# Performance work log

Measured on AMD Instinct MI355X. Metric: run time of the kernel, lower is better.

Reference implementation:

```python
import jax, jax.numpy as jnp
import numpy as np

N = 8192
F_IN = 128
N_META = 128
N_EMBED = 128


def setup_inputs() -> dict:
    key = jax.random.key(0)
    k1, k2, k3, k4, k5, k6 = jax.random.split(key, 6)
    X = jax.random.normal(k1, (N, F_IN), dtype=jnp.float32)
    A = jax.random.uniform(k2, (N, N), dtype=jnp.float32)  # dense nonneg adjacency
    s = 1.0 / np.sqrt(F_IN)
    W_embed = jax.random.uniform(k3, (N_EMBED, F_IN), dtype=jnp.float32, minval=-s, maxval=s)
    b_embed = jax.random.uniform(k4, (N_EMBED,), dtype=jnp.float32, minval=-s, maxval=s)
    W_assign = jax.random.uniform(k5, (N_META, F_IN), dtype=jnp.float32, minval=-s, maxval=s)
    b_assign = jax.random.uniform(k6, (N_META,), dtype=jnp.float32, minval=-s, maxval=s)
    return {"X": X, "A": A, "W_embed": W_embed, "b_embed": b_embed,
            "W_assign": W_assign, "b_assign": b_assign}


def reference(X, A, W_embed, b_embed, W_assign, b_assign):
    n = A.shape[0]
    # A_hat = A + I; symmetric normalization D^-1/2 A_hat D^-1/2.
    # (Original builds full diag matrices; result equals row/col scaling.)
    A_hat = A + jnp.eye(n, dtype=A.dtype)
    deg = jnp.sum(A_hat, axis=1)
    d_inv_sqrt = jnp.where(deg > 0, jax.lax.rsqrt(deg), 0.0)
    A_norm = d_inv_sqrt[:, None] * A_hat * d_inv_sqrt[None, :]
    AX = A_norm @ X  # shared by both GCN layers: [N, F]
    z_l = AX @ W_embed.T + b_embed                      # [N, n_embed]
    s_l = jax.nn.softmax(AX @ W_assign.T + b_assign, axis=-1)  # [N, n_meta]
    X_next = s_l.T @ z_l                                 # [n_meta, n_embed]
    A_next = s_l.T @ (A @ s_l)                           # [n_meta, n_meta]
    return (X_next, A_next, s_l)
```

## Files before the change

kernel.cpp:

```cpp
#include <hip/hip_runtime.h>
#include <hip/hip_bf16.h>
#include <cstdint>

typedef short v8s __attribute__((ext_vector_type(8)));
typedef float v4f __attribute__((ext_vector_type(4)));

#define DEV __device__ __forceinline__

DEV unsigned short f2bu(float f) {
  unsigned u = __builtin_bit_cast(unsigned, f);
  u += 0x7fffu + ((u >> 16) & 1u);
  return (unsigned short)(u >> 16);
}

DEV v8s pack8(const float4& a, const float4& b) {
  v8s r;
  r[0] = (short)f2bu(a.x); r[1] = (short)f2bu(a.y);
  r[2] = (short)f2bu(a.z); r[3] = (short)f2bu(a.w);
  r[4] = (short)f2bu(b.x); r[5] = (short)f2bu(b.y);
  r[6] = (short)f2bu(b.z); r[7] = (short)f2bu(b.w);
  return r;
}

template<bool CVT>
__global__ __launch_bounds__(256)
void k_degcvt(const float* __restrict__ A, float* __restrict__ dinv,
              unsigned short* __restrict__ Abf) {
  const int row = blockIdx.x;
  const float* ar = A + (size_t)row * 8192;
  unsigned short* aw = Abf + (size_t)row * 8192;
  float s = 0.f;
  #pragma unroll
  for (int i = 0; i < 8; ++i) {
    const int c = i * 1024 + threadIdx.x * 4;
    float4 v = *(const float4*)(ar + c);
    s += (v.x + v.y) + (v.z + v.w);
    if constexpr (CVT) {
      uint2 w;
      w.x = (unsigned)f2bu(v.x) | ((unsigned)f2bu(v.y) << 16);
      w.y = (unsigned)f2bu(v.z) | ((unsigned)f2bu(v.w) << 16);
      *(uint2*)(aw + c) = w;
    }
  }
  #pragma unroll
  for (int d = 1; d < 64; d <<= 1) s += __shfl_xor(s, d);
  __shared__ float wsum[4];
  if ((threadIdx.x & 63) == 0) wsum[threadIdx.x >> 6] = s;
  __syncthreads();
  if (threadIdx.x == 0) {
    dinv[row] = rsqrtf(1.0f + ((wsum[0] + wsum[1]) + (wsum[2] + wsum[3])));
  }
}

template<bool SCALE>
__global__ __launch_bounds__(256)
void k_transpose(const float* __restrict__ in, unsigned short* __restrict__ out,
                 const float* __restrict__ dinv) {
  __shared__ float tile[32][129];
  const int j0 = blockIdx.x * 32;
  const int t = threadIdx.x;
  const int r0 = t >> 5, sl = t & 31;
  #pragma unroll
  for (int i = 0; i < 4; ++i) {
    int r = r0 + i * 8;
    float4 v = *(const float4*)(in + (size_t)(j0 + r) * 128 + sl * 4);
    float sc = 1.0f;
    if constexpr (SCALE) sc = dinv[j0 + r];
    tile[r][sl * 4 + 0] = v.x * sc;
    tile[r][sl * 4 + 1] = v.y * sc;
    tile[r][sl * 4 + 2] = v.z * sc;
    tile[r][sl * 4 + 3] = v.w * sc;
  }
  __syncthreads();
  const int c = t >> 1, h = t & 1;
  unsigned short* op = out + (size_t)c * 8192 + j0 + h * 16;
  #pragma unroll
  for (int q = 0; q < 2; ++q) {
    int rb = h * 16 + q * 8;
    uint4 w;
    w.x = (unsigned)f2bu(tile[rb + 0][c]) | ((unsigned)f2bu(tile[rb + 1][c]) << 16);
    w.y = (unsigned)f2bu(tile[rb + 2][c]) | ((unsigned)f2bu(tile[rb + 3][c]) << 16);
    w.z = (unsigned)f2bu(tile[rb + 4][c]) | ((unsigned)f2bu(tile[rb + 5][c]) << 16);
    w.w = (unsigned)f2bu(tile[rb + 6][c]) | ((unsigned)f2bu(tile[rb + 7][c]) << 16);
    *(uint4*)(op + q * 8) = w;
  }
}

__global__ __launch_bounds__(512, 4)
void k_gemm_lds(const unsigned short* __restrict__ Ab16,
                const unsigned short* __restrict__ Bt, float* __restrict__ parts) {
  __shared__ alignas(16) char bsm[2][32768];
  const int t = threadIdx.x;
  const int wv = t >> 6, l = t & 63;
  const int rg = wv >> 1, wc = wv & 1;
  const int i0 = blockIdx.x * 128 + rg * 32;
  const int k0 = blockIdx.y * 1024;
  const int lr = l & 15, lq = l >> 4;

  const unsigned short* pA0 = Ab16 + (size_t)(i0 + lr) * 8192 + k0 + lq * 8;
  const unsigned short* pA1 = pA0 + (size_t)16 * 8192;

  const int sc = t >> 4, sk16 = t & 15;
  const unsigned short* pS = Bt + (size_t)sc * 8192 + k0 + sk16 * 8;
  int woff[4];
  #pragma unroll
  for (int i = 0; i < 4; ++i) {
    const int c = sc + i * 32;
    woff[i] = ((c << 8) + sk16 * 16) ^ ((c & 7) << 4);
  }

  v4f acc[2][4];
  #pragma unroll
  for (int mt = 0; mt < 2; ++mt)
    #pragma unroll
    for (int nt = 0; nt < 4; ++nt) acc[mt][nt] = (v4f){0.f, 0.f, 0.f, 0.f};

  v8s breg[4];
  v8s areg[2][4][2];

  auto stage_load = [&](int c) {
    #pragma unroll
    for (int i = 0; i < 4; ++i)
      breg[i] = *(const v8s*)(pS + (size_t)i * 32 * 8192 + c * 128);
  };
  auto stage_write = [&](int buf) {
    #pragma unroll
    for (int i = 0; i < 4; ++i)
      *(v8s*)(bsm[buf] + woff[i]) = breg[i];
  };

  stage_load(0);
  stage_write(0);
  #pragma unroll
  for (int kf = 0; kf < 4; ++kf) {
    areg[0][kf][0] = *(const v8s*)(pA0 + kf * 32);
    areg[0][kf][1] = *(const v8s*)(pA1 + kf * 32);
  }
  __syncthreads();

  #pragma unroll
  for (int c = 0; c < 8; ++c) {
    if (c < 7) {
      stage_load(c + 1);
      #pragma unroll
      for (int kf = 0; kf < 4; ++kf) {
        areg[(c + 1) & 1][kf][0] = *(const v8s*)(pA0 + (c + 1) * 128 + kf * 32);
        areg[(c + 1) & 1][kf][1] = *(const v8s*)(pA1 + (c + 1) * 128 + kf * 32);
      }
    }
    #pragma unroll
    for (int ks = 0; ks < 4; ++ks) {
      #pragma unroll
      for (int nt = 0; nt < 4; ++nt) {
        const int col = wc * 64 + nt * 16 + lr;
        const int off = (((col << 8) + ks * 64 + lq * 16) ^ ((col & 7) << 4));
        v8s bf = *(const v8s*)(bsm[c & 1] + off);
        acc[0][nt] = __builtin_amdgcn_mfma_f32_16x16x32_bf16(areg[c & 1][ks][0], bf, acc[0][nt], 0, 0, 0);
        acc[1][nt] = __builtin_amdgcn_mfma_f32_16x16x32_bf16(areg[c & 1][ks][1], bf, acc[1][nt], 0, 0, 0);
      }
    }
    if (c < 7) {
      stage_write((c + 1) & 1);
      __syncthreads();
    }
  }

  float* p = parts + (size_t)blockIdx.y * (8192 * 128);
  const int colb = wc * 64;
  #pragma unroll
  for (int mt = 0; mt < 2; ++mt)
    #pragma unroll
    for (int nt = 0; nt < 4; ++nt)
      #pragma unroll
      for (int r = 0; r < 4; ++r)
        p[(size_t)(i0 + mt * 16 + lq * 4 + r) * 128 + colb + nt * 16 + lr] = acc[mt][nt][r];
}

__global__ __launch_bounds__(512)
void k_gemm_f32(const float* __restrict__ Af, const unsigned short* __restrict__ Bt,
                float* __restrict__ parts) {
  constexpr int KSTEPS = 2048 / 32;
  const int t = threadIdx.x;
  const int wv = t >> 6, l = t & 63;
  const int rg = wv >> 1, ch = wv & 1;
  const int i0 = blockIdx.x * 128 + rg * 32;
  const int k0 = blockIdx.y * 2048;
  const int lr = l & 15, lk = (l >> 4) * 8;

  const float* pAf0 = Af + (size_t)(i0 + lr) * 8192 + k0 + lk;
  const float* pAf1 = pAf0 + (size_t)16 * 8192;
  const unsigned short* pB[4];
  #pragma unroll
  for (int nt = 0; nt < 4; ++nt)
    pB[nt] = Bt + (size_t)(ch * 64 + nt * 16 + lr) * 8192 + k0 + lk;

  v4f acc[2][4];
  #pragma unroll
  for (int mt = 0; mt < 2; ++mt)
    #pragma unroll
    for (int nt = 0; nt < 4; ++nt) acc[mt][nt] = (v4f){0.f, 0.f, 0.f, 0.f};

  float4 af_[2][2][2];
  v8s bb[2][4];

  auto loadab = [&](int buf, int k) {
    af_[buf][0][0] = *(const float4*)(pAf0 + k);
    af_[buf][0][1] = *(const float4*)(pAf0 + k + 4);
    af_[buf][1][0] = *(const float4*)(pAf1 + k);
    af_[buf][1][1] = *(const float4*)(pAf1 + k + 4);
    #pragma unroll
    for (int nt = 0; nt < 4; ++nt) bb[buf][nt] = *(const v8s*)(pB[nt] + k);
  };
  auto mfmas = [&](int buf) {
    #pragma unroll
    for (int mt = 0; mt < 2; ++mt) {
      v8s a_ = pack8(af_[buf][mt][0], af_[buf][mt][1]);
      #pragma unroll
      for (int nt = 0; nt < 4; ++nt)
        acc[mt][nt] = __builtin_amdgcn_mfma_f32_16x16x32_bf16(a_, bb[buf][nt], acc[mt][nt], 0, 0, 0);
    }
  };

  loadab(0, 0);
  for (int kt = 0; kt < KSTEPS; kt += 2) {
    loadab(1, (kt + 1) * 32);
    mfmas(0);
    if (kt + 2 < KSTEPS) loadab(0, (kt + 2) * 32);
    mfmas(1);
  }

  float* p = parts + (size_t)blockIdx.y * (8192 * 128);
  const int colb = ch * 64;
  #pragma unroll
  for (int mt = 0; mt < 2; ++mt)
    #pragma unroll
    for (int nt = 0; nt < 4; ++nt)
      #pragma unroll
      for (int r = 0; r < 4; ++r)
        p[(size_t)(i0 + mt * 16 + (l >> 4) * 4 + r) * 128 + colb + nt * 16 + lr] = acc[mt][nt][r];
}

__global__ __launch_bounds__(256)
void k_post1(const float* __restrict__ parts, int nsplit,
             const float* __restrict__ dinv, const float* __restrict__ Xg,
             const float* __restrict__ We, const float* __restrict__ be,
             const float* __restrict__ Wa, const float* __restrict__ ba,
             float* __restrict__ sl_out, unsigned short* __restrict__ slt,
             unsigned short* __restrict__ zlt) {
  __shared__ alignas(16) unsigned short axs[32 * 128];
  __shared__ float lg[32 * 128];
  __shared__ unsigned short sbf[32 * 130];
  __shared__ unsigned short zbf[32 * 130];
  const int t = threadIdx.x;
  const int i0 = blockIdx.x * 32;

  {
    const int r = t >> 3, cg = t & 7;
    const size_t base = (size_t)(i0 + r) * 128 + cg * 16;
    float acc[16];
    #pragma unroll
    for (int q = 0; q < 4; ++q) {
      float4 v = *(const float4*)(parts + base + q * 4);
      acc[q * 4 + 0] = v.x; acc[q * 4 + 1] = v.y;
      acc[q * 4 + 2] = v.z; acc[q * 4 + 3] = v.w;
    }
    for (int s = 1; s < nsplit; ++s) {
      #pragma unroll
      for (int q = 0; q < 4; ++q) {
        float4 v = *(const float4*)(parts + (size_t)s * 1048576 + base + q * 4);
        acc[q * 4 + 0] += v.x; acc[q * 4 + 1] += v.y;
        acc[q * 4 + 2] += v.z; acc[q * 4 + 3] += v.w;
      }
    }
    const float di = dinv[i0 + r];
    unsigned short bx[16];
    #pragma unroll
    for (int q = 0; q < 4; ++q) {
      float4 xv = *(const float4*)(Xg + base + q * 4);
      bx[q * 4 + 0] = f2bu(di * (acc[q * 4 + 0] + di * xv.x));
      bx[q * 4 + 1] = f2bu(di * (acc[q * 4 + 1] + di * xv.y));
      bx[q * 4 + 2] = f2bu(di * (acc[q * 4 + 2] + di * xv.z));
      bx[q * 4 + 3] = f2bu(di * (acc[q * 4 + 3] + di * xv.w));
    }
    char* Ab = (char*)axs;
    const int b0 = (r << 8) + cg * 32, sw = (r & 7) << 4;
    uint4 w0, w1;
    w0.x = (unsigned)bx[0] | ((unsigned)bx[1] << 16);
    w0.y = (unsigned)bx[2] | ((unsigned)bx[3] << 16);
    w0.z = (unsigned)bx[4] | ((unsigned)bx[5] << 16);
    w0.w = (unsigned)bx[6] | ((unsigned)bx[7] << 16);
    w1.x = (unsigned)bx[8] | ((unsigned)bx[9] << 16);
    w1.y = (unsigned)bx[10] | ((unsigned)bx[11] << 16);
    w1.z = (unsigned)bx[12] | ((unsigned)bx[13] << 16);
    w1.w = (unsigned)bx[14] | ((unsigned)bx[15] << 16);
    *(uint4*)(Ab + (b0 ^ sw)) = w0;
    *(uint4*)(Ab + ((b0 + 16) ^ sw)) = w1;
  }
  __syncthreads();

  const int wv = t >> 6, l = t & 63, fr = l & 15;
  {
    v4f zac[2][2], lac[2][2];
    #pragma unroll
    for (int a = 0; a < 2; ++a)
      #pragma unroll
      for (int b = 0; b < 2; ++b) {
        zac[a][b] = (v4f){0.f, 0.f, 0.f, 0.f};
        lac[a][b] = (v4f){0.f, 0.f, 0.f, 0.f};
      }
    const int kk = (l >> 4) * 8;
    #pragma unroll
    for (int ks = 0; ks < 4; ++ks) {
      const int k = ks * 32 + kk;
      #pragma unroll
      for (int nj = 0; nj < 2; ++nj) {
        const int col = nj * 64 + wv * 16 + fr;
        v8s bfe = pack8(*(const float4*)(We + col * 128 + k),
                        *(const float4*)(We + col * 128 + k + 4));
        v8s bfa = pack8(*(const float4*)(Wa + col * 128 + k),
                        *(const float4*)(Wa + col * 128 + k + 4));
        #pragma unroll
        for (int mt = 0; mt < 2; ++mt) {
          const int arow = mt * 16 + fr;
          v8s af = *(const v8s*)((char*)axs + (((arow << 8) + k * 2) ^ ((fr & 7) << 4)));
          zac[mt][nj] = __builtin_amdgcn_mfma_f32_16x16x32_bf16(af, bfe, zac[mt][nj], 0, 0, 0);
          lac[mt][nj] = __builtin_amdgcn_mfma_f32_16x16x32_bf16(af, bfa, lac[mt][nj], 0, 0, 0);
        }
      }
    }
    #pragma unroll
    for (int mt = 0; mt < 2; ++mt)
      #pragma unroll
      for (int nj = 0; nj < 2; ++nj)
        #pragma unroll
        for (int r4 = 0; r4 < 4; ++r4) {
          const int row = mt * 16 + (l >> 4) * 4 + r4;
          const int col = nj * 64 + wv * 16 + fr;
          lg[row * 128 + col] = lac[mt][nj][r4] + ba[col];
          zbf[row * 130 + col] = f2bu(zac[mt][nj][r4] + be[col]);
        }
  }
  __syncthreads();

  {
    const int r = t >> 3, g = t & 7;
    const float* lp = lg + r * 128 + g * 16;
    float x[16];
    #pragma unroll
    for (int q = 0; q < 4; ++q) {
      float4 v = *(const float4*)(lp + q * 4);
      x[q * 4 + 0] = v.x; x[q * 4 + 1] = v.y; x[q * 4 + 2] = v.z; x[q * 4 + 3] = v.w;
    }
    float mx = x[0];
    #pragma unroll
    for (int j = 1; j < 16; ++j) mx = fmaxf(mx, x[j]);
    #pragma unroll
    for (int d = 1; d < 8; d <<= 1) mx = fmaxf(mx, __shfl_xor(mx, d));
    float sum = 0.f;
    #pragma unroll
    for (int j = 0; j < 16; ++j) { x[j] = __expf(x[j] - mx); sum += x[j]; }
    #pragma unroll
    for (int d = 1; d < 8; d <<= 1) sum += __shfl_xor(sum, d);
    const float inv = 1.0f / sum;
    float* op = sl_out + (size_t)(i0 + r) * 128 + g * 16;
    #pragma unroll
    for (int q = 0; q < 4; ++q) {
      float4 o;
      o.x = x[q * 4 + 0] * inv; o.y = x[q * 4 + 1] * inv;
      o.z = x[q * 4 + 2] * inv; o.w = x[q * 4 + 3] * inv;
      *(float4*)(op + q * 4) = o;
    }
    #pragma unroll
    for (int j = 0; j < 16; ++j) sbf[r * 130 + g * 16 + j] = f2bu(x[j] * inv);
  }
  __syncthreads();

  {
    const int c = t & 127;
    const unsigned short* src = (t < 128) ? sbf : zbf;
    unsigned short* dst = (t < 128) ? slt : zlt;
    unsigned short* o = dst + (size_t)c * 8192 + i0;
    #pragma unroll
    for (int q = 0; q < 4; ++q) {
      uint4 w;
      w.x = (unsigned)src[(q * 8 + 0) * 130 + c] | ((unsigned)src[(q * 8 + 1) * 130 + c] << 16);
      w.y = (unsigned)src[(q * 8 + 2) * 130 + c] | ((unsigned)src[(q * 8 + 3) * 130 + c] << 16);
      w.z = (unsigned)src[(q * 8 + 4) * 130 + c] | ((unsigned)src[(q * 8 + 5) * 130 + c] << 16);
      w.w = (unsigned)src[(q * 8 + 6) * 130 + c] | ((unsigned)src[(q * 8 + 7) * 130 + c] << 16);
      *(uint4*)(o + q * 8) = w;
    }
  }
}

__global__ __launch_bounds__(256)
void k_post2(const float* __restrict__ parts, int nsplit, unsigned short* __restrict__ ast) {
  __shared__ unsigned short sb[32 * 130];
  const int t = threadIdx.x;
  const int i0 = blockIdx.x * 32;
  {
    const int r = t >> 3, cg = t & 7;
    const size_t base = (size_t)(i0 + r) * 128 + cg * 16;
    float acc[16];
    #pragma unroll
    for (int q = 0; q < 4; ++q) {
      float4 v = *(const float4*)(parts + base + q * 4);
      acc[q * 4 + 0] = v.x; acc[q * 4 + 1] = v.y;
      acc[q * 4 + 2] = v.z; acc[q * 4 + 3] = v.w;
    }
    for (int s = 1; s < nsplit; ++s) {
      #pragma unroll
      for (int q = 0; q < 4; ++q) {
        float4 v = *(const float4*)(parts + (size_t)s * 1048576 + base + q * 4);
        acc[q * 4 + 0] += v.x; acc[q * 4 + 1] += v.y;
        acc[q * 4 + 2] += v.z; acc[q * 4 + 3] += v.w;
      }
    }
    #pragma unroll
    for (int j = 0; j < 16; ++j) sb[r * 130 + cg * 16 + j] = f2bu(acc[j]);
  }
  __syncthreads();
  if (t < 128) {
    unsigned short* o = ast + (size_t)t * 8192 + i0;
    #pragma unroll
    for (int q = 0; q < 4; ++q) {
      uint4 w;
      w.x = (unsigned)sb[(q * 8 + 0) * 130 + t] | ((unsigned)sb[(q * 8 + 1) * 130 + t] << 16);
      w.y = (unsigned)sb[(q * 8 + 2) * 130 + t] | ((unsigned)sb[(q * 8 + 3) * 130 + t] << 16);
      w.z = (unsigned)sb[(q * 8 + 4) * 130 + t] | ((unsigned)sb[(q * 8 + 5) * 130 + t] << 16);
      w.w = (unsigned)sb[(q * 8 + 6) * 130 + t] | ((unsigned)sb[(q * 8 + 7) * 130 + t] << 16);
      *(uint4*)(o + q * 8) = w;
    }
  }
}

__global__ __launch_bounds__(256)
void k_outer(const unsigned short* __restrict__ slt, const unsigned short* __restrict__ zlt,
             const unsigned short* __restrict__ ast, float* __restrict__ parts) {
  const int t = threadIdx.x, wv = t >> 6, ln = t & 63;
  const int k0 = blockIdx.x * 128;
  const int lm = ln & 15, lk = (ln >> 4) << 3;
  v4f c1[2][8];
  v4f c2[2][8];
  #pragma unroll
  for (int mt = 0; mt < 2; ++mt)
    #pragma unroll
    for (int nt = 0; nt < 8; ++nt) { c1[mt][nt] = (v4f){0.f,0.f,0.f,0.f}; c2[mt][nt] = (v4f){0.f,0.f,0.f,0.f}; }
  #pragma unroll
  for (int ks = 0; ks < 4; ++ks) {
    int k = k0 + ks * 32 + lk;
    v8s a0 = *(const v8s*)(slt + (size_t)(wv * 32 + lm) * 8192 + k);
    v8s a1 = *(const v8s*)(slt + (size_t)(wv * 32 + 16 + lm) * 8192 + k);
    #pragma unroll
    for (int nt = 0; nt < 8; ++nt) {
      v8s bz = *(const v8s*)(zlt + (size_t)(nt * 16 + lm) * 8192 + k);
      v8s bs = *(const v8s*)(ast + (size_t)(nt * 16 + lm) * 8192 + k);
      c1[0][nt] = __builtin_amdgcn_mfma_f32_16x16x32_bf16(a0, bz, c1[0][nt], 0, 0, 0);
      c1[1][nt] = __builtin_amdgcn_mfma_f32_16x16x32_bf16(a1, bz, c1[1][nt], 0, 0, 0);
      c2[0][nt] = __builtin_amdgcn_mfma_f32_16x16x32_bf16(a0, bs, c2[0][nt], 0, 0, 0);
      c2[1][nt] = __builtin_amdgcn_mfma_f32_16x16x32_bf16(a1, bs, c2[1][nt], 0, 0, 0);
    }
  }
  float* p = parts + (size_t)blockIdx.x * 32768;
  #pragma unroll
  for (int mt = 0; mt < 2; ++mt)
    #pragma unroll
    for (int nt = 0; nt < 8; ++nt)
      #pragma unroll
      for (int r = 0; r < 4; ++r) {
        int m = wv * 32 + mt * 16 + ((ln >> 4) << 2) + r;
        int n = nt * 16 + lm;
        p[m * 128 + n] = c1[mt][nt][r];
        p[16384 + m * 128 + n] = c2[mt][nt][r];
      }
}

__global__ __launch_bounds__(256)
void k_reduce(const float* __restrict__ parts, float* __restrict__ out) {
  const int o = blockIdx.x * 256 + threadIdx.x;
  float s = 0.f;
  for (int b = 0; b < 64; ++b) s += parts[(size_t)b * 32768 + o];
  out[o] = s;
}

extern "C" void kernel_launch(void* const* d_in, const int* in_sizes, int n_in,
                              void* d_out, int out_size, void* d_ws, size_t ws_size,
                              hipStream_t stream) {
  (void)in_sizes; (void)n_in; (void)out_size;
  const float* X  = (const float*)d_in[0];
  const float* A  = (const float*)d_in[1];
  const float* We = (const float*)d_in[2];
  const float* be = (const float*)d_in[3];
  const float* Wa = (const float*)d_in[4];
  const float* ba = (const float*)d_in[5];
  float* out = (float*)d_out;
  float* sl = out + 32768;

  char* ws = (char*)d_ws;
  constexpr size_t OFF_XPT  = 32768;
  constexpr size_t OFF_SLT  = OFF_XPT + 2097152;
  constexpr size_t OFF_ZLT  = OFF_SLT + 2097152;
  constexpr size_t OFF_AST  = OFF_ZLT + 2097152;
  constexpr size_t OFF_PART = OFF_AST + 2097152;
  constexpr size_t OFF_ABF  = OFF_PART + 67108864;
  constexpr size_t NEED_ABF = OFF_ABF + 134217728ull;

  float*          dinv = (float*)(ws + 0);
  unsigned short* xpt  = (unsigned short*)(ws + OFF_XPT);
  unsigned short* slt  = (unsigned short*)(ws + OFF_SLT);
  unsigned short* zlt  = (unsigned short*)(ws + OFF_ZLT);
  unsigned short* ast  = (unsigned short*)(ws + OFF_AST);
  float*          part = (float*)(ws + OFF_PART);
  unsigned short* abfp = (unsigned short*)(ws + OFF_ABF);

  const bool abf = ws_size >= NEED_ABF;
  const int  sk  = abf ? 8 : 4;

  if (abf) k_degcvt<true><<<8192, 256, 0, stream>>>(A, dinv, abfp);
  else     k_degcvt<false><<<8192, 256, 0, stream>>>(A, dinv, abfp);

  k_transpose<true><<<256, 256, 0, stream>>>(X, xpt, dinv);

  if (abf) k_gemm_lds<<<dim3(64, 8), 512, 0, stream>>>(abfp, xpt, part);
  else     k_gemm_f32<<<dim3(64, 4), 512, 0, stream>>>(A, xpt, part);

  k_post1<<<256, 256, 0, stream>>>(part, sk, dinv, X, We, be, Wa, ba, sl, slt, zlt);

  if (abf) k_gemm_lds<<<dim3(64, 8), 512, 0, stream>>>(abfp, slt, part);
  else     k_gemm_f32<<<dim3(64, 4), 512, 0, stream>>>(A, slt, part);

  k_post2<<<256, 256, 0, stream>>>(part, sk, ast);
  k_outer<<<64, 256, 0, stream>>>(slt, zlt, ast, part);
  k_reduce<<<128, 256, 0, stream>>>(part, out);
}
```

Baseline: 203.8 us.

## Fuse split-K reduction and post-processing into GEMM via last-block atomic counter

The split-K GEMM now writes its partial sums as bf16 instead of fp32. An atomic counter per row-block picks the last finishing K-slice block, and that block reduces the eight partials and runs the epilogue in place: the dense projections, softmax and transposed stores for the first GEMM, and the transposed A·s store for the second. This removes the separate post1/post2 launches and halves the partial-sum traffic. In exchange, the epilogue runs on only 64 blocks, LDS use grows, and the bf16 partials add rounding error.

```diff
diff --git a/kernel.cpp b/kernel.cpp
--- a/kernel.cpp
+++ b/kernel.cpp
@@ -11,6 +11,10 @@
   unsigned u = __builtin_bit_cast(unsigned, f);
   u += 0x7fffu + ((u >> 16) & 1u);
   return (unsigned short)(u >> 16);
+}
+
+DEV float bu2f(unsigned short u) {
+  return __builtin_bit_cast(float, ((unsigned)u) << 16);
 }
 
 DEV v8s pack8(const float4& a, const float4& b) {
@@ -25,7 +29,8 @@
 template<bool CVT>
 __global__ __launch_bounds__(256)
 void k_degcvt(const float* __restrict__ A, float* __restrict__ dinv,
-              unsigned short* __restrict__ Abf) {
+              unsigned short* __restrict__ Abf, unsigned* __restrict__ cnt) {
+  if (blockIdx.x == 0 && threadIdx.x < 128) cnt[threadIdx.x] = 0;
   const int row = blockIdx.x;
   const float* ar = A + (size_t)row * 8192;
   unsigned short* aw = Abf + (size_t)row * 8192;
@@ -86,10 +91,20 @@
   }
 }
 
+template<int EPI>
 __global__ __launch_bounds__(512, 4)
 void k_gemm_lds(const unsigned short* __restrict__ Ab16,
-                const unsigned short* __restrict__ Bt, float* __restrict__ parts) {
-  __shared__ alignas(16) char bsm[2][32768];
+                const unsigned short* __restrict__ Bt,
+                unsigned short* __restrict__ parts, unsigned* __restrict__ cnt,
+                const float* __restrict__ dinv, const float* __restrict__ Xg,
+                const float* __restrict__ We, const float* __restrict__ be,
+                const float* __restrict__ Wa, const float* __restrict__ ba,
+                float* __restrict__ sl_out, unsigned short* __restrict__ slt,
+                unsigned short* __restrict__ zlt, unsigned short* __restrict__ ast) {
+  __shared__ alignas(16) char smem[66560];
+  __shared__ int lastf;
+  char* bsm0 = smem;
+  char* bsm1 = smem + 32768;
   const int t = threadIdx.x;
   const int wv = t >> 6, l = t & 63;
   const int rg = wv >> 1, wc = wv & 1;
@@ -123,14 +138,14 @@
     for (int i = 0; i < 4; ++i)
       breg[i] = *(const v8s*)(pS + (size_t)i * 32 * 8192 + c * 128);
   };
-  auto stage_write = [&](int buf) {
+  auto stage_write = [&](char* buf) {
     #pragma unroll
     for (int i = 0; i < 4; ++i)
-      *(v8s*)(bsm[buf] + woff[i]) = breg[i];
+      *(v8s*)(buf + woff[i]) = breg[i];
   };
 
   stage_load(0);
-  stage_write(0);
+  stage_write(bsm0);
   #pragma unroll
   for (int kf = 0; kf < 4; ++kf) {
     areg[0][kf][0] = *(const v8s*)(pA0 + kf * 32);
@@ -148,32 +163,218 @@
         areg[(c + 1) & 1][kf][1] = *(const v8s*)(pA1 + (c + 1) * 128 + kf * 32);
       }
     }
+    char* bcur = (c & 1) ? bsm1 : bsm0;
     #pragma unroll
     for (int ks = 0; ks < 4; ++ks) {
       #pragma unroll
       for (int nt = 0; nt < 4; ++nt) {
         const int col = wc * 64 + nt * 16 + lr;
         const int off = (((col << 8) + ks * 64 + lq * 16) ^ ((col & 7) << 4));
-        v8s bf = *(const v8s*)(bsm[c & 1] + off);
+        v8s bf = *(const v8s*)(bcur + off);
         acc[0][nt] = __builtin_amdgcn_mfma_f32_16x16x32_bf16(areg[c & 1][ks][0], bf, acc[0][nt], 0, 0, 0);
         acc[1][nt] = __builtin_amdgcn_mfma_f32_16x16x32_bf16(areg[c & 1][ks][1], bf, acc[1][nt], 0, 0, 0);
       }
     }
     if (c < 7) {
-      stage_write((c + 1) & 1);
+      stage_write((c & 1) ? bsm0 : bsm1);
       __syncthreads();
     }
   }
 
-  float* p = parts + (size_t)blockIdx.y * (8192 * 128);
-  const int colb = wc * 64;
-  #pragma unroll
-  for (int mt = 0; mt < 2; ++mt)
-    #pragma unroll
-    for (int nt = 0; nt < 4; ++nt)
-      #pragma unroll
-      for (int r = 0; r < 4; ++r)
-        p[(size_t)(i0 + mt * 16 + lq * 4 + r) * 128 + colb + nt * 16 + lr] = acc[mt][nt][r];
+  {
+    unsigned short* p = parts + (size_t)blockIdx.y * (8192 * 128);
+    const int colb = wc * 64;
+    #pragma unroll
+    for (int mt = 0; mt < 2; ++mt)
+      #pragma unroll
+      for (int nt = 0; nt < 4; ++nt)
+        #pragma unroll
+        for (int r = 0; r < 4; ++r)
+          p[(size_t)(i0 + mt * 16 + lq * 4 + r) * 128 + colb + nt * 16 + lr] = f2bu(acc[mt][nt][r]);
+  }
+
+  __threadfence();
+  if (t == 0) {
+    unsigned old = atomicAdd(&cnt[blockIdx.x], 1u);
+    lastf = (old == 7);
+  }
+  __syncthreads();
+  if (!lastf) return;
+  __threadfence();
+
+  const int i0g = blockIdx.x * 128;
+
+  if constexpr (EPI == 1) {
+    unsigned short* axs  = (unsigned short*)smem;
+    unsigned short* tbuf = (unsigned short*)(smem + 32768);
+
+    {
+      const int r = t >> 2, cg = t & 3;
+      const int gr = i0g + r;
+      float sacc[32];
+      #pragma unroll
+      for (int j = 0; j < 32; ++j) sacc[j] = 0.f;
+      for (int y = 0; y < 8; ++y) {
+        const unsigned short* pp = parts + (size_t)y * 1048576 + (size_t)gr * 128 + cg * 32;
+        #pragma unroll
+        for (int q = 0; q < 4; ++q) {
+          v8s v = *(const v8s*)(pp + q * 8);
+          #pragma unroll
+          for (int j = 0; j < 8; ++j)
+            sacc[q * 8 + j] += bu2f((unsigned short)v[j]);
+        }
+      }
+      const float di = dinv[gr];
+      const float* xp = Xg + (size_t)gr * 128 + cg * 32;
+      unsigned short ax[32];
+      #pragma unroll
+      for (int q = 0; q < 8; ++q) {
+        float4 xv = *(const float4*)(xp + q * 4);
+        ax[q * 4 + 0] = f2bu(di * (sacc[q * 4 + 0] + di * xv.x));
+        ax[q * 4 + 1] = f2bu(di * (sacc[q * 4 + 1] + di * xv.y));
+        ax[q * 4 + 2] = f2bu(di * (sacc[q * 4 + 2] + di * xv.z));
+        ax[q * 4 + 3] = f2bu(di * (sacc[q * 4 + 3] + di * xv.w));
+      }
+      char* axb = (char*)axs;
+      #pragma unroll
+      for (int u = 0; u < 4; ++u) {
+        uint4 w;
+        w.x = (unsigned)ax[u * 8 + 0] | ((unsigned)ax[u * 8 + 1] << 16);
+        w.y = (unsigned)ax[u * 8 + 2] | ((unsigned)ax[u * 8 + 3] << 16);
+        w.z = (unsigned)ax[u * 8 + 4] | ((unsigned)ax[u * 8 + 5] << 16);
+        w.w = (unsigned)ax[u * 8 + 6] | ((unsigned)ax[u * 8 + 7] << 16);
+        *(uint4*)(axb + (((r << 8) + cg * 64 + u * 16) ^ ((r & 7) << 4))) = w;
+      }
+    }
+    __syncthreads();
+
+    const int rb = wv * 16;
+    v4f zac[8], lac[8];
+    #pragma unroll
+    for (int nj = 0; nj < 8; ++nj) {
+      zac[nj] = (v4f){0.f, 0.f, 0.f, 0.f};
+      lac[nj] = (v4f){0.f, 0.f, 0.f, 0.f};
+    }
+    const char* axb = (const char*)axs;
+    #pragma unroll
+    for (int ks = 0; ks < 4; ++ks) {
+      const int k = ks * 32 + lq * 8;
+      const int arow = rb + lr;
+      v8s af = *(const v8s*)(axb + ((((arow) << 8) + k * 2) ^ ((lr & 7) << 4)));
+      #pragma unroll
+      for (int nj = 0; nj < 8; ++nj) {
+        const int cb = nj * 16 + lr;
+        v8s bfe = pack8(*(const float4*)(We + cb * 128 + k),
+                        *(const float4*)(We + cb * 128 + k + 4));
+        v8s bfa = pack8(*(const float4*)(Wa + cb * 128 + k),
+                        *(const float4*)(Wa + cb * 128 + k + 4));
+        zac[nj] = __builtin_amdgcn_mfma_f32_16x16x32_bf16(af, bfe, zac[nj], 0, 0, 0);
+        lac[nj] = __builtin_amdgcn_mfma_f32_16x16x32_bf16(af, bfa, lac[nj], 0, 0, 0);
+      }
+    }
+    #pragma unroll
+    for (int nj = 0; nj < 8; ++nj) {
+      const float bav = ba[nj * 16 + lr];
+      const float bev = be[nj * 16 + lr];
+      #pragma unroll
+      for (int r4 = 0; r4 < 4; ++r4) { lac[nj][r4] += bav; zac[nj][r4] += bev; }
+    }
+
+    #pragma unroll
+    for (int r4 = 0; r4 < 4; ++r4) {
+      float mx = lac[0][r4];
+      #pragma unroll
+      for (int nj = 1; nj < 8; ++nj) mx = fmaxf(mx, lac[nj][r4]);
+      #pragma unroll
+      for (int d = 1; d < 16; d <<= 1) mx = fmaxf(mx, __shfl_xor(mx, d));
+      float e[8], sum = 0.f;
+      #pragma unroll
+      for (int nj = 0; nj < 8; ++nj) { e[nj] = __expf(lac[nj][r4] - mx); sum += e[nj]; }
+      #pragma unroll
+      for (int d = 1; d < 16; d <<= 1) sum += __shfl_xor(sum, d);
+      const float inv = 1.0f / sum;
+      const int row = rb + lq * 4 + r4;
+      float* op = sl_out + (size_t)(i0g + row) * 128 + lr;
+      #pragma unroll
+      for (int nj = 0; nj < 8; ++nj) {
+        const float s = e[nj] * inv;
+        op[nj * 16] = s;
+        tbuf[row * 130 + nj * 16 + lr] = f2bu(s);
+      }
+    }
+    __syncthreads();
+
+    if (t < 128) {
+      unsigned short* o = slt + (size_t)t * 8192 + i0g;
+      #pragma unroll
+      for (int q = 0; q < 16; ++q) {
+        uint4 w;
+        w.x = (unsigned)tbuf[(q * 8 + 0) * 130 + t] | ((unsigned)tbuf[(q * 8 + 1) * 130 + t] << 16);
+        w.y = (unsigned)tbuf[(q * 8 + 2) * 130 + t] | ((unsigned)tbuf[(q * 8 + 3) * 130 + t] << 16);
+        w.z = (unsigned)tbuf[(q * 8 + 4) * 130 + t] | ((unsigned)tbuf[(q * 8 + 5) * 130 + t] << 16);
+        w.w = (unsigned)tbuf[(q * 8 + 6) * 130 + t] | ((unsigned)tbuf[(q * 8 + 7) * 130 + t] << 16);
+        *(uint4*)(o + q * 8) = w;
+      }
+    }
+    __syncthreads();
+
+    #pragma unroll
+    for (int nj = 0; nj < 8; ++nj)
+      #pragma unroll
+      for (int r4 = 0; r4 < 4; ++r4) {
+        const int row = rb + lq * 4 + r4;
+        tbuf[row * 130 + nj * 16 + lr] = f2bu(zac[nj][r4]);
+      }
+    __syncthreads();
+
+    if (t < 128) {
+      unsigned short* o = zlt + (size_t)t * 8192 + i0g;
+      #pragma unroll
+      for (int q = 0; q < 16; ++q) {
+        uint4 w;
+        w.x = (unsigned)tbuf[(q * 8 + 0) * 130 + t] | ((unsigned)tbuf[(q * 8 + 1) * 130 + t] << 16);
+        w.y = (unsigned)tbuf[(q * 8 + 2) * 130 + t] | ((unsigned)tbuf[(q * 8 + 3) * 130 + t] << 16);
+        w.z = (unsigned)tbuf[(q * 8 + 4) * 130 + t] | ((unsigned)tbuf[(q * 8 + 5) * 130 + t] << 16);
+        w.w = (unsigned)tbuf[(q * 8 + 6) * 130 + t] | ((unsigned)tbuf[(q * 8 + 7) * 130 + t] << 16);
+        *(uint4*)(o + q * 8) = w;
+      }
+    }
+  } else {
+    unsigned short* tbuf = (unsigned short*)smem;
+    {
+      const int r = t >> 2, cg = t & 3;
+      const int gr = i0g + r;
+      float sacc[32];
+      #pragma unroll
+      for (int j = 0; j < 32; ++j) sacc[j] = 0.f;
+      for (int y = 0; y < 8; ++y) {
+        const unsigned short* pp = parts + (size_t)y * 1048576 + (size_t)gr * 128 + cg * 32;
+        #pragma unroll
+        for (int q = 0; q < 4; ++q) {
+          v8s v = *(const v8s*)(pp + q * 8);
+          #pragma unroll
+          for (int j = 0; j < 8; ++j)
+            sacc[q * 8 + j] += bu2f((unsigned short)v[j]);
+        }
+      }
+      #pragma unroll
+      for (int j = 0; j < 32; ++j)
+        tbuf[r * 130 + cg * 32 + j] = f2bu(sacc[j]);
+    }
+    __syncthreads();
+    if (t < 128) {
+      unsigned short* o = ast + (size_t)t * 8192 + i0g;
+      #pragma unroll
+      for (int q = 0; q < 16; ++q) {
+        uint4 w;
+        w.x = (unsigned)tbuf[(q * 8 + 0) * 130 + t] | ((unsigned)tbuf[(q * 8 + 1) * 130 + t] << 16);
+        w.y = (unsigned)tbuf[(q * 8 + 2) * 130 + t] | ((unsigned)tbuf[(q * 8 + 3) * 130 + t] << 16);
+        w.z = (unsigned)tbuf[(q * 8 + 4) * 130 + t] | ((unsigned)tbuf[(q * 8 + 5) * 130 + t] << 16);
+        w.w = (unsigned)tbuf[(q * 8 + 6) * 130 + t] | ((unsigned)tbuf[(q * 8 + 7) * 130 + t] << 16);
+        *(uint4*)(o + q * 8) = w;
+      }
+    }
+  }
 }
 
 __global__ __launch_bounds__(512)
@@ -501,34 +702,42 @@
   constexpr size_t OFF_ZLT  = OFF_SLT + 2097152;
   constexpr size_t OFF_AST  = OFF_ZLT + 2097152;
   constexpr size_t OFF_PART = OFF_AST + 2097152;
+  constexpr size_t OFF_CNT  = OFF_PART + 33554432;
   constexpr size_t OFF_ABF  = OFF_PART + 67108864;
   constexpr size_t NEED_ABF = OFF_ABF + 134217728ull;
 
-  float*          dinv = (float*)(ws + 0);
-  unsigned short* xpt  = (unsigned short*)(ws + OFF_XPT);
-  unsigned short* slt  = (unsigned short*)(ws + OFF_SLT);
-  unsigned short* zlt  = (unsigned short*)(ws + OFF_ZLT);
-  unsigned short* ast  = (unsigned short*)(ws + OFF_AST);
-  float*          part = (float*)(ws + OFF_PART);
-  unsigned short* abfp = (unsigned short*)(ws + OFF_ABF);
+  float*          dinv  = (float*)(ws + 0);
+  unsigned short* xpt   = (unsigned short*)(ws + OFF_XPT);
+  unsigned short* slt   = (unsigned short*)(ws + OFF_SLT);
+  unsigned short* zlt   = (unsigned short*)(ws + OFF_ZLT);
+  unsigned short* ast   = (unsigned short*)(ws + OFF_AST);
+  float*          partf = (float*)(ws + OFF_PART);
+  unsigned short* partb = (unsigned short*)(ws + OFF_PART);
+  unsigned*       cnt   = (unsigned*)(ws + OFF_CNT);
+  unsigned short* abfp  = (unsigned short*)(ws + OFF_ABF);
 
   const bool abf = ws_size >= NEED_ABF;
-  const int  sk  = abf ? 8 : 4;
-
-  if (abf) k_degcvt<true><<<8192, 256, 0, stream>>>(A, dinv, abfp);
-  else     k_degcvt<false><<<8192, 256, 0, stream>>>(A, dinv, abfp);
+
+  if (abf) k_degcvt<true><<<8192, 256, 0, stream>>>(A, dinv, abfp, cnt);
+  else     k_degcvt<false><<<8192, 256, 0, stream>>>(A, dinv, abfp, cnt);
 
   k_transpose<true><<<256, 256, 0, stream>>>(X, xpt, dinv);
 
-  if (abf) k_gemm_lds<<<dim3(64, 8), 512, 0, stream>>>(abfp, xpt, part);
-  else     k_gemm_f32<<<dim3(64, 4), 512, 0, stream>>>(A, xpt, part);
-
-  k_post1<<<256, 256, 0, stream>>>(part, sk, dinv, X, We, be, Wa, ba, sl, slt, zlt);
-
-  if (abf) k_gemm_lds<<<dim3(64, 8), 512, 0, stream>>>(abfp, slt, part);
-  else     k_gemm_f32<<<dim3(64, 4), 512, 0, stream>>>(A, slt, part);
-
-  k_post2<<<256, 256, 0, stream>>>(part, sk, ast);
-  k_outer<<<64, 256, 0, stream>>>(slt, zlt, ast, part);
-  k_reduce<<<128, 256, 0, stream>>>(part, out);
-}
+  if (abf) {
+    k_gemm_lds<1><<<dim3(64, 8), 512, 0, stream>>>(abfp, xpt, partb, cnt,
+                                                   dinv, X, We, be, Wa, ba,
+                                                   sl, slt, zlt, nullptr);
+    k_gemm_lds<2><<<dim3(64, 8), 512, 0, stream>>>(abfp, slt, partb, cnt + 64,
+                                                   nullptr, nullptr, nullptr, nullptr,
+                                                   nullptr, nullptr, nullptr, nullptr,
+                                                   nullptr, ast);
+  } else {
+    k_gemm_f32<<<dim3(64, 4), 512, 0, stream>>>(A, xpt, partf);
+    k_post1<<<256, 256, 0, stream>>>(partf, 4, dinv, X, We, be, Wa, ba, sl, slt, zlt);
+    k_gemm_f32<<<dim3(64, 4), 512, 0, stream>>>(A, slt, partf);
+    k_post2<<<256, 256, 0, stream>>>(partf, 4, ast);
+  }
+
+  k_outer<<<64, 256, 0, stream>>>(slt, zlt, ast, partf);
+  k_reduce<<<128, 256, 0, stream>>>(partf, out);
+}
```

Result: slower. 570.8 us (+180.0%).
